# Kernel optimization log

Measured on AMD Instinct MI355X. Metric: run time of the kernel, lower is better.

## Reference

```python
import jax, jax.numpy as jnp
import numpy as np

K = 3          # kernel_size
PAD = 1        # padding
HEADS = 4
C = 128
K2 = K * K


def setup_inputs() -> dict:
    key = jax.random.key(0)
    k1, k2, k3, k4 = jax.random.split(key, 4)
    B, H, W = 4, 128, 128
    x = jax.random.normal(k1, (B, H, W, C), jnp.float32)
    w_qkv = jax.random.normal(k2, (K2 * K2 * HEADS, C), jnp.float32) * 0.02
    w_v = jax.random.normal(k3, (K2, C, C), jnp.float32) * np.sqrt(2.0 / (K2 * C))
    w_proj = jax.random.normal(k4, (C, C), jnp.float32) * 0.02
    return {"x": x, "w_qkv": w_qkv, "w_v": w_v, "w_proj": w_proj}


def _csa(x, w_qkv, w_v, w_proj):
    B, H, W, Cc = x.shape
    hd = Cc // HEADS
    scale = hd ** (-0.5)
    N = H * W
    # attention map: Linear(C -> k^4*heads); pool is identity for stride=1
    att = jnp.einsum('bhwc,oc->bhwo', x, w_qkv)                      # [B,H,W,81*heads]
    att = att.reshape(B, N, HEADS, K2, K2).transpose(0, 2, 1, 3, 4)  # [B,heads,N,k2,k2]
    att = jax.nn.softmax(att * scale, axis=-1)
    # unfold x into per-location 3x3 windows (patch index p = di*K + dj)
    xp = jnp.pad(x, ((0, 0), (PAD, PAD), (PAD, PAD), (0, 0)))
    patches = jnp.stack([xp[:, di:di + H, dj:dj + W, :]
                         for di in range(K) for dj in range(K)], axis=3)  # [B,H,W,k2,C]
    v = patches.reshape(B, N, K2, Cc)
    # grouped 1x1 conv == per-window-position CxC matmul
    v = jnp.einsum('pij,bnpj->bnpi', w_v, v)                          # [B,N,k2,C]
    v = v.reshape(B, N, K2, HEADS, hd).transpose(0, 3, 1, 2, 4)       # [B,heads,N,k2,hd]
    out = jnp.einsum('bhnpq,bhnqd->bhnpd', att, v)                    # [B,heads,N,k2,hd]
    # -> [B, C, k2, H, W] with channel index = head*hd + d (matches torch fold layout)
    out = out.transpose(0, 1, 4, 3, 2).reshape(B, Cc, K2, H, W)
    # fold: scatter-add overlapping patches back to (H, W)
    acc = jnp.zeros((B, Cc, H + 2 * PAD, W + 2 * PAD), x.dtype)
    p = 0
    for di in range(K):
        for dj in range(K):
            acc = acc.at[:, :, di:di + H, dj:dj + W].add(out[:, :, p])
            p += 1
    y = acc[:, :, PAD:PAD + H, PAD:PAD + W].transpose(0, 2, 3, 1)     # [B,H,W,C]
    return jnp.einsum('bhwc,oc->bhwo', y, w_proj)


def reference(x, w_qkv, w_v, w_proj):
    return _csa(x, w_qkv, w_v, w_proj)
```

## Files before the change

### kernel.cpp

```cpp
#include <hip/hip_runtime.h>


typedef short bf16x8 __attribute__((ext_vector_type(8)));
typedef float f32x4  __attribute__((ext_vector_type(4)));
typedef float v2f    __attribute__((ext_vector_type(2)));

#define SCALE 0.17677669529663687f

__device__ __forceinline__ unsigned short f2bf(float f) {
  unsigned u = __float_as_uint(f);
  u = (u + 0x7fffu + ((u >> 16) & 1u)) >> 16;
  return (unsigned short)u;
}
__device__ __forceinline__ float bf2f(unsigned short s) {
  return __uint_as_float(((unsigned)s) << 16);
}
__device__ __forceinline__ unsigned pk2bf(float lo, float hi) {
  unsigned a = __float_as_uint(lo) + 0x8000u;
  unsigned b = __float_as_uint(hi) + 0x8000u;
  return __builtin_amdgcn_perm(b, a, 0x07060302u);
}
__device__ __forceinline__ bf16x8 ld16(const unsigned short* p) {
  union { bf16x8 v; uint4 u; } r;
  r.u = *(const uint4*)p;
  return r.v;
}

__global__ __launch_bounds__(256) void cvt_kernel(const float* __restrict__ wq,
                                                  const float* __restrict__ wv,
                                                  const float* __restrict__ wp,
                                                  unsigned short* __restrict__ wqb,
                                                  unsigned short* __restrict__ wvb,
                                                  unsigned short* __restrict__ wpb) {
  long i = ((long)blockIdx.x * 256 + threadIdx.x) * 4;
  if (i >= 205312) return;
  const float* src; unsigned short* dst; long off;
  if (i < 41472)       { src = wq; dst = wqb; off = i; }
  else if (i < 188928) { src = wv; dst = wvb; off = i - 41472; }
  else                 { src = wp; dst = wpb; off = i - 188928; }
  float4 v = *(const float4*)(src + off);
  ushort4 o;
  o.x = f2bf(v.x); o.y = f2bf(v.y); o.z = f2bf(v.z); o.w = f2bf(v.w);
  *(ushort4*)(dst + off) = o;
}

__global__ __launch_bounds__(256) void att_kernel(const float* __restrict__ x,
                                                  const unsigned short* __restrict__ wqb,
                                                  unsigned* __restrict__ attb) {
  __shared__ unsigned short A[64 * 136];
  __shared__ unsigned short Bl[96 * 136];
  __shared__ float lg[64][84];
  const int t = threadIdx.x;
  const long m0 = (long)blockIdx.x * 64;
#pragma unroll
  for (int k = 0; k < 8; k++) {
    int i = t + k * 256;
    int row = i >> 5, seg = i & 31;
    float4 v = *(const float4*)(x + (m0 + row) * 128 + seg * 4);
    *(uint2*)((unsigned*)A + row * 68 + seg * 2) =
        make_uint2(pk2bf(v.x, v.y), pk2bf(v.z, v.w));
  }
  const int wv = t >> 6, lane = t & 63, qd = lane >> 4, l15 = lane & 15;
  __syncthreads();
  bf16x8 af[4];
#pragma unroll
  for (int kk = 0; kk < 4; kk++)
    af[kk] = ld16(A + (wv * 16 + l15) * 136 + kk * 32 + qd * 8);

  unsigned short* attile = Bl;
  for (int h = 0; h < 4; h++) {
    __syncthreads();
    for (int i = t; i < 1296; i += 256) {
      int row = i >> 4, seg = i & 15;
      const uint4 v = *(const uint4*)(wqb + (long)(h * 81 + row) * 128 + seg * 8);
      *(uint4*)((unsigned*)Bl + row * 68 + seg * 4) = v;
    }
    __syncthreads();
    f32x4 acc[6] = {};
#pragma unroll
    for (int kk = 0; kk < 4; kk++)
#pragma unroll
      for (int tn = 0; tn < 6; tn++) {
        bf16x8 bf = ld16(Bl + (tn * 16 + l15) * 136 + kk * 32 + qd * 8);
        acc[tn] = __builtin_amdgcn_mfma_f32_16x16x32_bf16(af[kk], bf, acc[tn], 0, 0, 0);
      }
#pragma unroll
    for (int tn = 0; tn < 6; tn++)
#pragma unroll
      for (int r = 0; r < 4; r++) {
        int col = tn * 16 + l15;
        if (col < 81) lg[wv * 16 + qd * 4 + r][col] = acc[tn][r];
      }
    __syncthreads();
    for (int g = t; g < 576; g += 256) {
      int row = g / 9, p = g % 9;
      const float* L = &lg[row][p * 9];
      float mx = L[0];
#pragma unroll
      for (int q = 1; q < 9; q++) mx = fmaxf(mx, L[q]);
      float e[9], s = 0.f;
#pragma unroll
      for (int q = 0; q < 9; q++) { e[q] = __expf((L[q] - mx) * SCALE); s += e[q]; }
      float inv = 1.f / s;
#pragma unroll
      for (int q = 0; q < 9; q++) attile[row * 90 + q * 10 + p] = f2bf(e[q] * inv);
    }
    __syncthreads();
#pragma unroll
    for (int k = 0; k < 12; k++) {
      int i = t + k * 256;
      if (i < 2880) {
        int q = i / 320, rem = i - q * 320, n = rem / 5, j = rem - n * 5;
        attb[((size_t)(q * 4 + h) * 65536 + m0 + n) * 5 + j] =
            ((const unsigned*)attile)[n * 45 + q * 5 + j];
      }
    }
  }
}

__global__ __launch_bounds__(256, 2) void av_kernel(const float* __restrict__ x,
                                                    const unsigned short* __restrict__ wvb,
                                                    const unsigned* __restrict__ attb,
                                                    const unsigned short* __restrict__ wpb,
                                                    float* __restrict__ out) {
  __shared__ unsigned short A[144 * 136];
  __shared__ unsigned short S[100 * 136];
  __shared__ unsigned aLs[2400];
  const int t = threadIdx.x;
  const int bb = blockIdx.z;
  const int r0 = blockIdx.y * 8, c0 = blockIdx.x * 8;
  const int l15 = t & 15, qd = (t >> 4) & 3, wvi = t >> 6;
  const int n = wvi * 16 + l15, lr = n >> 3, lc = n & 7;
  const long nb = (long)bb * 16384;
  unsigned* Sdw = (unsigned*)S;
  unsigned* Adw = (unsigned*)A;

  int mlr_[7], mlc_[7];
#pragma unroll
  for (int nt = 0; nt < 7; nt++) {
    int ml = nt * 16 + l15;
    mlr_[nt] = ml / 10; mlc_[nt] = ml % 10;
  }

#pragma unroll
  for (int k = 0; k < 18; k++) {
    int i = t + k * 256;
    int row = i >> 5, seg = i & 31;
    int gr = r0 - 2 + row / 12, gc = c0 - 2 + row % 12;
    float4 v = make_float4(0.f, 0.f, 0.f, 0.f);
    if (gr >= 0 && gr < 128 && gc >= 0 && gc < 128)
      v = *(const float4*)(x + (nb + gr * 128 + gc) * 128 + seg * 4);
    *(uint2*)(Adw + row * 68 + seg * 2) = make_uint2(pk2bf(v.x, v.y), pk2bf(v.z, v.w));
  }

  v2f y2[16];
#pragma unroll
  for (int i = 0; i < 16; i++) y2[i] = (v2f){0.f, 0.f};

  unsigned avv[8];
  bf16x8 wvf[2][4];

#define LOAD_A(qq)                                                                        \
  {                                                                                       \
    _Pragma("unroll") for (int k = 0; k < 8; k++) {                                       \
      int i = t + k * 256;                                                                \
      if (i < 2000) {                                                                     \
        int hh = i / 500, rem = i - hh * 500, row = rem / 5, j5 = rem - row * 5;          \
        int gr = r0 - 1 + row / 10, gc = c0 - 1 + row % 10;                               \
        avv[k] = (gr >= 0 && gr < 128 && gc >= 0 && gc < 128)                             \
                     ? attb[((size_t)((qq) * 4 + hh) * 65536 + nb + gr * 128 + gc) * 5 +  \
                            j5]                                                           \
                     : 0u;                                                                \
      }                                                                                   \
    }                                                                                     \
  }
#define LOAD_WV(qq)                                                                       \
  {                                                                                       \
    _Pragma("unroll") for (int m = 0; m < 2; m++)                                         \
    _Pragma("unroll") for (int kk = 0; kk < 4; kk++)                                      \
      wvf[m][kk] = *(const bf16x8*)(wvb + ((size_t)(qq) * 128 + (wvi * 2 + m) * 16 +      \
                                           l15) * 128 + kk * 32 + qd * 8);                \
  }

  LOAD_A(0)
  LOAD_WV(0)

  for (int q = 0; q < 9; q++) {
    const int oqr = q / 3 - 1, oqc = q % 3 - 1;
    __syncthreads();

#pragma unroll
    for (int k = 0; k < 8; k++) {
      int i = t + k * 256;
      if (i < 2000) {
        int hh = i / 500, rem = i - hh * 500, row = rem / 5, j5 = rem - row * 5;
        aLs[hh * 600 + row * 6 + j5] = avv[k];
      }
    }

    f32x4 acc[2][7];
#pragma unroll
    for (int m = 0; m < 2; m++)
#pragma unroll
      for (int nt = 0; nt < 7; nt++) acc[m][nt] = (f32x4){0.f, 0.f, 0.f, 0.f};
#pragma unroll
    for (int nt = 0; nt < 7; nt++) {
      int xr = (mlr_[nt] + oqr + 1) * 12 + (mlc_[nt] + oqc + 1);
      xr = xr > 143 ? 143 : xr;
      bf16x8 bx[4];
#pragma unroll
      for (int kk = 0; kk < 4; kk++)
        bx[kk] = ld16(A + xr * 136 + kk * 32 + qd * 8);
#pragma unroll
      for (int m = 0; m < 2; m++)
#pragma unroll
        for (int kk = 0; kk < 4; kk++)
          acc[m][nt] = __builtin_amdgcn_mfma_f32_16x16x32_bf16(wvf[m][kk], bx[kk],
                                                               acc[m][nt], 0, 0, 0);
    }
#pragma unroll
    for (int m = 0; m < 2; m++)
#pragma unroll
      for (int nt = 0; nt < 7; nt++) {
        int loc = nt * 16 + l15;
        if (loc < 100) {
          int mt = wvi * 2 + m;
          *(uint2*)(Sdw + loc * 68 + mt * 8 + qd * 2) =
              make_uint2(pk2bf(acc[m][nt][0], acc[m][nt][1]),
                         pk2bf(acc[m][nt][2], acc[m][nt][3]));
        }
      }
    __syncthreads();
    if (q < 8) { LOAD_A(q + 1) LOAD_WV(q + 1) }

    const unsigned short* aS = (const unsigned short*)aLs;
#pragma unroll
    for (int p = 0; p < 9; p++) {
      const int em = 1 - p / 3, ec = 1 - p % 3;
      const int ml = (lr + em + 1) * 10 + (lc + ec + 1);
      const float a = bf2f(aS[qd * 1200 + ml * 12 + p]);
      const v2f a2 = {a, a};
      const uint4* Sr = (const uint4*)(Sdw + ml * 68 + (qd << 4));
#pragma unroll
      for (int v4 = 0; v4 < 4; v4++) {
        const uint4 u = Sr[v4];
        v2f xv;
        const int yi = v4 * 4;
        xv.x = __uint_as_float(u.x << 16); xv.y = __uint_as_float(u.x & 0xffff0000u);
        y2[yi + 0] += a2 * xv;
        xv.x = __uint_as_float(u.y << 16); xv.y = __uint_as_float(u.y & 0xffff0000u);
        y2[yi + 1] += a2 * xv;
        xv.x = __uint_as_float(u.z << 16); xv.y = __uint_as_float(u.z & 0xffff0000u);
        y2[yi + 2] += a2 * xv;
        xv.x = __uint_as_float(u.w << 16); xv.y = __uint_as_float(u.w & 0xffff0000u);
        y2[yi + 3] += a2 * xv;
      }
    }
  }

  __syncthreads();
  unsigned short* yb = A;
  {
    uint4 pk[4];
#pragma unroll
    for (int v4 = 0; v4 < 4; v4++) {
      pk[v4].x = pk2bf(y2[v4 * 4 + 0].x, y2[v4 * 4 + 0].y);
      pk[v4].y = pk2bf(y2[v4 * 4 + 1].x, y2[v4 * 4 + 1].y);
      pk[v4].z = pk2bf(y2[v4 * 4 + 2].x, y2[v4 * 4 + 2].y);
      pk[v4].w = pk2bf(y2[v4 * 4 + 3].x, y2[v4 * 4 + 3].y);
    }
    uint4* dst = (uint4*)(Adw + n * 68 + (qd << 4));
#pragma unroll
    for (int v4 = 0; v4 < 4; v4++) dst[v4] = pk[v4];
  }
  __syncthreads();
  f32x4 pacc[8] = {};
#pragma unroll
  for (int kk = 0; kk < 4; kk++) {
    bf16x8 afr = ld16(yb + (wvi * 16 + l15) * 136 + kk * 32 + qd * 8);
#pragma unroll
    for (int tn = 0; tn < 8; tn++) {
      bf16x8 bfr = *(const bf16x8*)(wpb + (tn * 16 + l15) * 128 + kk * 32 + qd * 8);
      pacc[tn] = __builtin_amdgcn_mfma_f32_16x16x32_bf16(afr, bfr, pacc[tn], 0, 0, 0);
    }
  }
#pragma unroll
  for (int tn = 0; tn < 8; tn++)
#pragma unroll
    for (int r = 0; r < 4; r++) {
      int nl = wvi * 16 + qd * 4 + r;
      int col = tn * 16 + l15;
      out[(nb + (r0 + (nl >> 3)) * 128 + (c0 + (nl & 7))) * 128 + col] = pacc[tn][r];
    }
}

extern "C" void kernel_launch(void* const* d_in, const int* in_sizes, int n_in,
                              void* d_out, int out_size, void* d_ws, size_t ws_size,
                              hipStream_t stream) {
  const float* x  = (const float*)d_in[0];
  const float* wq = (const float*)d_in[1];
  const float* wv = (const float*)d_in[2];
  const float* wp = (const float*)d_in[3];
  char* w = (char*)d_ws;
  unsigned*       attb = (unsigned*)w;
  unsigned short* wqb  = (unsigned short*)(w + 47185920);
  unsigned short* wvb  = wqb + 41472;
  unsigned short* wpb  = wvb + 147456;

  cvt_kernel<<<201, 256, 0, stream>>>(wq, wv, wp, wqb, wvb, wpb);
  att_kernel<<<1024, 256, 0, stream>>>(x, wqb, attb);
  dim3 g3(16, 16, 4);
  av_kernel<<<g3, 256, 0, stream>>>(x, wvb, attb, wpb, (float*)d_out);
}
```

Measured before the change: 214.2 us.

## Double threads per block in attention and AV kernels, splitting work across eight waves

Both the attention-map kernel and the fused AV/projection kernel now launch 512 threads instead of 256. Each wave takes half of the previous per-wave work: half of the output column tiles, or one MFMA row tile, or half of the channel groups. Index arithmetic for global stores and loads is precomputed once outside the head and window loops. The aim is more waves per CU for latency hiding with fewer registers per thread. The cost is more threads sharing the same LDS tiles and barriers, and in the AV kernel the activation tile loads are duplicated across wave pairs.

```diff
diff --git a/kernel.cpp b/kernel.cpp
--- a/kernel.cpp
+++ b/kernel.cpp
@@ -44,81 +44,95 @@
   *(ushort4*)(dst + off) = o;
 }
 
-__global__ __launch_bounds__(256) void att_kernel(const float* __restrict__ x,
-                                                  const unsigned short* __restrict__ wqb,
-                                                  unsigned* __restrict__ attb) {
+__device__ __forceinline__ void softmax9(const float* L, unsigned short* attile,
+                                         int row, int p) {
+  float mx = L[0];
+#pragma unroll
+  for (int q = 1; q < 9; q++) mx = fmaxf(mx, L[q]);
+  float e[9], s = 0.f;
+#pragma unroll
+  for (int q = 0; q < 9; q++) { e[q] = __expf((L[q] - mx) * SCALE); s += e[q]; }
+  float inv = 1.f / s;
+#pragma unroll
+  for (int q = 0; q < 9; q++) attile[row * 90 + q * 10 + p] = f2bf(e[q] * inv);
+}
+
+__global__ __launch_bounds__(512, 4) void att_kernel(const float* __restrict__ x,
+                                                     const unsigned short* __restrict__ wqb,
+                                                     unsigned* __restrict__ attb) {
   __shared__ unsigned short A[64 * 136];
   __shared__ unsigned short Bl[96 * 136];
   __shared__ float lg[64][84];
   const int t = threadIdx.x;
   const long m0 = (long)blockIdx.x * 64;
 #pragma unroll
-  for (int k = 0; k < 8; k++) {
-    int i = t + k * 256;
+  for (int k = 0; k < 4; k++) {
+    int i = t + k * 512;
     int row = i >> 5, seg = i & 31;
     float4 v = *(const float4*)(x + (m0 + row) * 128 + seg * 4);
     *(uint2*)((unsigned*)A + row * 68 + seg * 2) =
         make_uint2(pk2bf(v.x, v.y), pk2bf(v.z, v.w));
   }
-  const int wv = t >> 6, lane = t & 63, qd = lane >> 4, l15 = lane & 15;
+  const int w = t >> 6, lane = t & 63, qd = lane >> 4, l15 = lane & 15;
+  const int rw = w & 3, th = w >> 2;
+  const int sr0 = t / 9, sp0 = t - sr0 * 9;
+  const int sr1 = (t + 512) / 9, sp1 = (t + 512) - sr1 * 9;
+  int dsto[6], srco[6];
+#pragma unroll
+  for (int k = 0; k < 6; k++) {
+    int i = t + k * 512;
+    if (i < 2880) {
+      int q = i / 320, rem = i - q * 320, n = rem / 5, j = rem - n * 5;
+      dsto[k] = (int)(((size_t)(q * 4) * 65536 + m0 + n) * 5 + j);
+      srco[k] = n * 45 + q * 5 + j;
+    } else { dsto[k] = -1; srco[k] = 0; }
+  }
   __syncthreads();
   bf16x8 af[4];
 #pragma unroll
   for (int kk = 0; kk < 4; kk++)
-    af[kk] = ld16(A + (wv * 16 + l15) * 136 + kk * 32 + qd * 8);
+    af[kk] = ld16(A + (rw * 16 + l15) * 136 + kk * 32 + qd * 8);
 
   unsigned short* attile = Bl;
   for (int h = 0; h < 4; h++) {
     __syncthreads();
-    for (int i = t; i < 1296; i += 256) {
-      int row = i >> 4, seg = i & 15;
-      const uint4 v = *(const uint4*)(wqb + (long)(h * 81 + row) * 128 + seg * 8);
-      *(uint4*)((unsigned*)Bl + row * 68 + seg * 4) = v;
-    }
-    __syncthreads();
-    f32x4 acc[6] = {};
+#pragma unroll
+    for (int k = 0; k < 3; k++) {
+      int i = t + k * 512;
+      if (i < 1296) {
+        int row = i >> 4, seg = i & 15;
+        const uint4 v = *(const uint4*)(wqb + (long)(h * 81 + row) * 128 + seg * 8);
+        *(uint4*)((unsigned*)Bl + row * 68 + seg * 4) = v;
+      }
+    }
+    __syncthreads();
+    f32x4 acc[3] = {};
 #pragma unroll
     for (int kk = 0; kk < 4; kk++)
 #pragma unroll
-      for (int tn = 0; tn < 6; tn++) {
-        bf16x8 bf = ld16(Bl + (tn * 16 + l15) * 136 + kk * 32 + qd * 8);
+      for (int tn = 0; tn < 3; tn++) {
+        bf16x8 bf = ld16(Bl + ((th * 3 + tn) * 16 + l15) * 136 + kk * 32 + qd * 8);
         acc[tn] = __builtin_amdgcn_mfma_f32_16x16x32_bf16(af[kk], bf, acc[tn], 0, 0, 0);
       }
 #pragma unroll
-    for (int tn = 0; tn < 6; tn++)
+    for (int tn = 0; tn < 3; tn++)
 #pragma unroll
       for (int r = 0; r < 4; r++) {
-        int col = tn * 16 + l15;
-        if (col < 81) lg[wv * 16 + qd * 4 + r][col] = acc[tn][r];
+        int col = (th * 3 + tn) * 16 + l15;
+        if (col < 81) lg[rw * 16 + qd * 4 + r][col] = acc[tn][r];
       }
     __syncthreads();
-    for (int g = t; g < 576; g += 256) {
-      int row = g / 9, p = g % 9;
-      const float* L = &lg[row][p * 9];
-      float mx = L[0];
-#pragma unroll
-      for (int q = 1; q < 9; q++) mx = fmaxf(mx, L[q]);
-      float e[9], s = 0.f;
-#pragma unroll
-      for (int q = 0; q < 9; q++) { e[q] = __expf((L[q] - mx) * SCALE); s += e[q]; }
-      float inv = 1.f / s;
-#pragma unroll
-      for (int q = 0; q < 9; q++) attile[row * 90 + q * 10 + p] = f2bf(e[q] * inv);
-    }
-    __syncthreads();
-#pragma unroll
-    for (int k = 0; k < 12; k++) {
-      int i = t + k * 256;
-      if (i < 2880) {
-        int q = i / 320, rem = i - q * 320, n = rem / 5, j = rem - n * 5;
-        attb[((size_t)(q * 4 + h) * 65536 + m0 + n) * 5 + j] =
-            ((const unsigned*)attile)[n * 45 + q * 5 + j];
-      }
-    }
-  }
-}
-
-__global__ __launch_bounds__(256, 2) void av_kernel(const float* __restrict__ x,
+    softmax9(&lg[sr0][sp0 * 9], attile, sr0, sp0);
+    if (t < 64) softmax9(&lg[sr1][sp1 * 9], attile, sr1, sp1);
+    __syncthreads();
+#pragma unroll
+    for (int k = 0; k < 6; k++)
+      if (dsto[k] >= 0)
+        attb[dsto[k] + h * 327680] = ((const unsigned*)attile)[srco[k]];
+  }
+}
+
+__global__ __launch_bounds__(512, 4) void av_kernel(const float* __restrict__ x,
                                                     const unsigned short* __restrict__ wvb,
                                                     const unsigned* __restrict__ attb,
                                                     const unsigned short* __restrict__ wpb,
@@ -130,21 +144,22 @@
   const int bb = blockIdx.z;
   const int r0 = blockIdx.y * 8, c0 = blockIdx.x * 8;
   const int l15 = t & 15, qd = (t >> 4) & 3, wvi = t >> 6;
-  const int n = wvi * 16 + l15, lr = n >> 3, lc = n & 7;
+  const int n = (wvi & 3) * 16 + l15, lr = n >> 3, lc = n & 7;
+  const int g = (wvi >> 2) * 4 + qd, head = g >> 1;
   const long nb = (long)bb * 16384;
   unsigned* Sdw = (unsigned*)S;
   unsigned* Adw = (unsigned*)A;
 
-  int mlr_[7], mlc_[7];
+  int xbase_[7];
 #pragma unroll
   for (int nt = 0; nt < 7; nt++) {
     int ml = nt * 16 + l15;
-    mlr_[nt] = ml / 10; mlc_[nt] = ml % 10;
-  }
-
-#pragma unroll
-  for (int k = 0; k < 18; k++) {
-    int i = t + k * 256;
+    xbase_[nt] = (ml / 10) * 12 + (ml % 10) + 13;
+  }
+
+#pragma unroll
+  for (int k = 0; k < 9; k++) {
+    int i = t + k * 512;
     int row = i >> 5, seg = i & 31;
     int gr = r0 - 2 + row / 12, gc = c0 - 2 + row % 12;
     float4 v = make_float4(0.f, 0.f, 0.f, 0.f);
@@ -153,96 +168,83 @@
     *(uint2*)(Adw + row * 68 + seg * 2) = make_uint2(pk2bf(v.x, v.y), pk2bf(v.z, v.w));
   }
 
-  v2f y2[16];
-#pragma unroll
-  for (int i = 0; i < 16; i++) y2[i] = (v2f){0.f, 0.f};
-
-  unsigned avv[8];
-  bf16x8 wvf[2][4];
-
-#define LOAD_A(qq)                                                                        \
-  {                                                                                       \
-    _Pragma("unroll") for (int k = 0; k < 8; k++) {                                       \
-      int i = t + k * 256;                                                                \
-      if (i < 2000) {                                                                     \
-        int hh = i / 500, rem = i - hh * 500, row = rem / 5, j5 = rem - row * 5;          \
-        int gr = r0 - 1 + row / 10, gc = c0 - 1 + row % 10;                               \
-        avv[k] = (gr >= 0 && gr < 128 && gc >= 0 && gc < 128)                             \
-                     ? attb[((size_t)((qq) * 4 + hh) * 65536 + nb + gr * 128 + gc) * 5 +  \
-                            j5]                                                           \
-                     : 0u;                                                                \
-      }                                                                                   \
-    }                                                                                     \
-  }
-#define LOAD_WV(qq)                                                                       \
-  {                                                                                       \
-    _Pragma("unroll") for (int m = 0; m < 2; m++)                                         \
-    _Pragma("unroll") for (int kk = 0; kk < 4; kk++)                                      \
-      wvf[m][kk] = *(const bf16x8*)(wvb + ((size_t)(qq) * 128 + (wvi * 2 + m) * 16 +      \
-                                           l15) * 128 + kk * 32 + qd * 8);                \
-  }
+  int aoff[4], aidx[4];
+#pragma unroll
+  for (int k = 0; k < 4; k++) {
+    int i = t + k * 512;
+    if (i < 2000) {
+      int hh = i / 500, rem = i - hh * 500, row = rem / 5, j5 = rem - row * 5;
+      int gr = r0 - 1 + row / 10, gc = c0 - 1 + row % 10;
+      aidx[k] = hh * 600 + row * 6 + j5;
+      aoff[k] = (gr >= 0 && gr < 128 && gc >= 0 && gc < 128)
+                    ? (int)(((size_t)hh * 65536 + nb + gr * 128 + gc) * 5 + j5)
+                    : -1;
+    } else { aidx[k] = -1; aoff[k] = -1; }
+  }
+  const unsigned short* pwv = wvb + (size_t)(wvi * 16 + l15) * 128 + qd * 8;
+
+  v2f y2[8];
+#pragma unroll
+  for (int i = 0; i < 8; i++) y2[i] = (v2f){0.f, 0.f};
+
+  unsigned avv[4];
+  bf16x8 wvf[4];
+
+#define LOAD_A(qq)                                                              \
+  { _Pragma("unroll") for (int k = 0; k < 4; k++)                               \
+      avv[k] = (aoff[k] >= 0) ? attb[aoff[k] + (qq) * 1310720] : 0u; }
+#define LOAD_WV(qq)                                                             \
+  { _Pragma("unroll") for (int kk = 0; kk < 4; kk++)                            \
+      wvf[kk] = *(const bf16x8*)(pwv + (size_t)(qq) * 16384 + kk * 32); }
 
   LOAD_A(0)
   LOAD_WV(0)
 
   for (int q = 0; q < 9; q++) {
-    const int oqr = q / 3 - 1, oqc = q % 3 - 1;
-    __syncthreads();
-
-#pragma unroll
-    for (int k = 0; k < 8; k++) {
-      int i = t + k * 256;
-      if (i < 2000) {
-        int hh = i / 500, rem = i - hh * 500, row = rem / 5, j5 = rem - row * 5;
-        aLs[hh * 600 + row * 6 + j5] = avv[k];
-      }
-    }
-
-    f32x4 acc[2][7];
-#pragma unroll
-    for (int m = 0; m < 2; m++)
-#pragma unroll
-      for (int nt = 0; nt < 7; nt++) acc[m][nt] = (f32x4){0.f, 0.f, 0.f, 0.f};
+    const int qoff = (q / 3) * 12 + (q % 3) - 13;
+    __syncthreads();
+
+#pragma unroll
+    for (int k = 0; k < 4; k++)
+      if (aidx[k] >= 0) aLs[aidx[k]] = avv[k];
+
+    f32x4 acc[7];
+#pragma unroll
+    for (int nt = 0; nt < 7; nt++) acc[nt] = (f32x4){0.f, 0.f, 0.f, 0.f};
 #pragma unroll
     for (int nt = 0; nt < 7; nt++) {
-      int xr = (mlr_[nt] + oqr + 1) * 12 + (mlc_[nt] + oqc + 1);
+      int xr = xbase_[nt] + qoff;
       xr = xr > 143 ? 143 : xr;
       bf16x8 bx[4];
 #pragma unroll
       for (int kk = 0; kk < 4; kk++)
         bx[kk] = ld16(A + xr * 136 + kk * 32 + qd * 8);
 #pragma unroll
-      for (int m = 0; m < 2; m++)
-#pragma unroll
-        for (int kk = 0; kk < 4; kk++)
-          acc[m][nt] = __builtin_amdgcn_mfma_f32_16x16x32_bf16(wvf[m][kk], bx[kk],
-                                                               acc[m][nt], 0, 0, 0);
-    }
-#pragma unroll
-    for (int m = 0; m < 2; m++)
-#pragma unroll
-      for (int nt = 0; nt < 7; nt++) {
-        int loc = nt * 16 + l15;
-        if (loc < 100) {
-          int mt = wvi * 2 + m;
-          *(uint2*)(Sdw + loc * 68 + mt * 8 + qd * 2) =
-              make_uint2(pk2bf(acc[m][nt][0], acc[m][nt][1]),
-                         pk2bf(acc[m][nt][2], acc[m][nt][3]));
-        }
-      }
+      for (int kk = 0; kk < 4; kk++)
+        acc[nt] = __builtin_amdgcn_mfma_f32_16x16x32_bf16(wvf[kk], bx[kk],
+                                                          acc[nt], 0, 0, 0);
+    }
+#pragma unroll
+    for (int nt = 0; nt < 7; nt++) {
+      int loc = nt * 16 + l15;
+      if (loc < 100)
+        *(uint2*)(Sdw + loc * 68 + wvi * 8 + qd * 2) =
+            make_uint2(pk2bf(acc[nt][0], acc[nt][1]),
+                       pk2bf(acc[nt][2], acc[nt][3]));
+    }
     __syncthreads();
     if (q < 8) { LOAD_A(q + 1) LOAD_WV(q + 1) }
 
     const unsigned short* aS = (const unsigned short*)aLs;
+    const int mlb = lr * 10 + lc + 11;
 #pragma unroll
     for (int p = 0; p < 9; p++) {
-      const int em = 1 - p / 3, ec = 1 - p % 3;
-      const int ml = (lr + em + 1) * 10 + (lc + ec + 1);
-      const float a = bf2f(aS[qd * 1200 + ml * 12 + p]);
+      const int ml = mlb + (1 - p / 3) * 10 + (1 - p % 3);
+      const float a = bf2f(aS[head * 1200 + ml * 12 + p]);
       const v2f a2 = {a, a};
-      const uint4* Sr = (const uint4*)(Sdw + ml * 68 + (qd << 4));
-#pragma unroll
-      for (int v4 = 0; v4 < 4; v4++) {
+      const uint4* Sr = (const uint4*)(Sdw + ml * 68 + g * 8);
+#pragma unroll
+      for (int v4 = 0; v4 < 2; v4++) {
         const uint4 u = Sr[v4];
         v2f xv;
         const int yi = v4 * 4;
@@ -261,35 +263,35 @@
   __syncthreads();
   unsigned short* yb = A;
   {
-    uint4 pk[4];
-#pragma unroll
-    for (int v4 = 0; v4 < 4; v4++) {
+    uint4 pk[2];
+#pragma unroll
+    for (int v4 = 0; v4 < 2; v4++) {
       pk[v4].x = pk2bf(y2[v4 * 4 + 0].x, y2[v4 * 4 + 0].y);
       pk[v4].y = pk2bf(y2[v4 * 4 + 1].x, y2[v4 * 4 + 1].y);
       pk[v4].z = pk2bf(y2[v4 * 4 + 2].x, y2[v4 * 4 + 2].y);
       pk[v4].w = pk2bf(y2[v4 * 4 + 3].x, y2[v4 * 4 + 3].y);
     }
-    uint4* dst = (uint4*)(Adw + n * 68 + (qd << 4));
-#pragma unroll
-    for (int v4 = 0; v4 < 4; v4++) dst[v4] = pk[v4];
+    uint4* dst = (uint4*)(Adw + n * 68 + g * 8);
+    dst[0] = pk[0]; dst[1] = pk[1];
   }
   __syncthreads();
-  f32x4 pacc[8] = {};
+  f32x4 pacc[4] = {};
 #pragma unroll
   for (int kk = 0; kk < 4; kk++) {
-    bf16x8 afr = ld16(yb + (wvi * 16 + l15) * 136 + kk * 32 + qd * 8);
-#pragma unroll
-    for (int tn = 0; tn < 8; tn++) {
-      bf16x8 bfr = *(const bf16x8*)(wpb + (tn * 16 + l15) * 128 + kk * 32 + qd * 8);
+    bf16x8 afr = ld16(yb + ((wvi & 3) * 16 + l15) * 136 + kk * 32 + qd * 8);
+#pragma unroll
+    for (int tn = 0; tn < 4; tn++) {
+      bf16x8 bfr = *(const bf16x8*)(wpb + (((wvi >> 2) * 4 + tn) * 16 + l15) * 128 +
+                                    kk * 32 + qd * 8);
       pacc[tn] = __builtin_amdgcn_mfma_f32_16x16x32_bf16(afr, bfr, pacc[tn], 0, 0, 0);
     }
   }
 #pragma unroll
-  for (int tn = 0; tn < 8; tn++)
+  for (int tn = 0; tn < 4; tn++)
 #pragma unroll
     for (int r = 0; r < 4; r++) {
-      int nl = wvi * 16 + qd * 4 + r;
-      int col = tn * 16 + l15;
+      int nl = (wvi & 3) * 16 + qd * 4 + r;
+      int col = ((wvi >> 2) * 4 + tn) * 16 + l15;
       out[(nb + (r0 + (nl >> 3)) * 128 + (c0 + (nl & 7))) * 128 + col] = pacc[tn][r];
     }
 }
@@ -308,7 +310,7 @@
   unsigned short* wpb  = wvb + 147456;
 
   cvt_kernel<<<201, 256, 0, stream>>>(wq, wv, wp, wqb, wvb, wpb);
-  att_kernel<<<1024, 256, 0, stream>>>(x, wqb, attb);
+  att_kernel<<<1024, 512, 0, stream>>>(x, wqb, attb);
   dim3 g3(16, 16, 4);
-  av_kernel<<<g3, 256, 0, stream>>>(x, wvb, attb, wpb, (float*)d_out);
-}
+  av_kernel<<<g3, 512, 0, stream>>>(x, wvb, attb, wpb, (float*)d_out);
+}
```

Measured after the change: 205.5 us. 1.04x faster.
